# Optimization experiments

Hardware: AMD Instinct MI355X
Metric: run time of the kernel (lower is better)

Reference implementation:

```python
import jax, jax.numpy as jnp
import numpy as np


def ste_sign(w):
    # straight-through binarization: forward sign(w), backward identity
    return w + jax.lax.stop_gradient(jnp.sign(w) - w)


def spike(x):
    # Heaviside spike with straight-through estimator
    return x + jax.lax.stop_gradient((x > 0).astype(x.dtype) - x)


def quantized_conv1d(x, w, b, stride, padding):
    # XNOR-Net style 1-bit weights: sign(w) * per-out-channel mean(|w|)
    alpha = jnp.mean(jnp.abs(w), axis=(1, 2), keepdims=True)  # (O,1,1)
    wq = ste_sign(w) * alpha
    y = jax.lax.conv_general_dilated(
        x, wq, window_strides=(stride,), padding=[(padding, padding)],
        dimension_numbers=('NCH', 'OIH', 'NCH'))
    return y + b[None, :, None]


def batchnorm(x, gamma, beta, eps=1e-5):
    # training-mode BN over (batch, length) per channel
    mu = jnp.mean(x, axis=(0, 2), keepdims=True)
    var = jnp.var(x, axis=(0, 2), keepdims=True)
    return (x - mu) * jax.lax.rsqrt(var + eps) * gamma[None, :, None] + beta[None, :, None]


def window_attn(sq, sk, sv, w):
    # spiking attention restricted to non-overlapping windows of size w
    B, L, C = sq.shape
    pad = (-L) % w
    p = lambda a: jnp.pad(a, ((0, 0), (0, pad), (0, 0)))  # zero-pad -> zero spikes
    q = p(sq).reshape(B, -1, w, C)
    k = p(sk).reshape(B, -1, w, C)
    v = p(sv).reshape(B, -1, w, C)
    attn = jnp.einsum('bnwc,bnuc->bnwu', q, k)           # (B, nW, w, w)
    out = jnp.einsum('bnwu,bnuc->bnwc', attn, v) / w
    return out.reshape(B, -1, C)[:, :L]


def global_attn(sq, K, V, g):
    # pool K,V down to g global tokens, then linear spiking attention
    B, L, C = K.shape
    chunk = -(-L // g)
    pad = chunk * g - L
    p = lambda a: jnp.pad(a, ((0, 0), (0, pad), (0, 0)))
    kp = p(K).reshape(B, g, chunk, C).mean(axis=2)       # (B, g, C)
    vp = p(V).reshape(B, g, chunk, C).mean(axis=2)
    skg, svg = spike(kp), spike(vp)
    kv = jnp.einsum('bgc,bgd->bcd', skg, svg)            # (B, C, C)
    return jnp.einsum('blc,bcd->bld', sq, kv) / g


def mssa(x, wq, wk, wv, wo, local_w=64, regional_w=256, global_pool=16):
    # x: (B, C, L) -> token-major (B, L, C)
    h = jnp.swapaxes(x, 1, 2)
    Q, K, V = h @ wq, h @ wk, h @ wv
    sq, sk, sv = spike(Q), spike(K), spike(V)
    out = (window_attn(sq, sk, sv, local_w)
           + window_attn(sq, sk, sv, regional_w)
           + global_attn(sq, K, V, global_pool)) / 3.0
    y = h + out @ wo  # residual
    return jnp.swapaxes(y, 1, 2)


def setup_inputs() -> dict:
    key = jax.random.key(0)
    ks = jax.random.split(key, 8)
    B, Cin, L, Cout = 32, 256, 5000, 128
    return {
        'x': jax.random.normal(ks[0], (B, Cin, L), jnp.float32),
        'conv_w': jax.random.normal(ks[1], (Cout, Cin, 9), jnp.float32) * 0.05,
        'conv_b': jnp.zeros((Cout,), jnp.float32),
        'gamma': jnp.ones((Cout,), jnp.float32),
        'beta': jnp.zeros((Cout,), jnp.float32),
        'wq': jax.random.normal(ks[2], (Cout, Cout), jnp.float32) * 0.09,
        'wk': jax.random.normal(ks[3], (Cout, Cout), jnp.float32) * 0.09,
        'wv': jax.random.normal(ks[4], (Cout, Cout), jnp.float32) * 0.09,
        'wo': jax.random.normal(ks[5], (Cout, Cout), jnp.float32) * 0.09,
    }


def reference(x, conv_w, conv_b, gamma, beta, wq, wk, wv, wo):
    y = quantized_conv1d(x, conv_w, conv_b, stride=2, padding=4)  # (B,128,2500)
    y = jax.nn.elu(batchnorm(y, gamma, beta))
    return mssa(y, wq, wk, wv, wo)                                # (B,128,2500)
```

## Files before the change

### kernel.cpp

```cpp
#include <hip/hip_runtime.h>

typedef __attribute__((ext_vector_type(8))) short bf16x8;
typedef __attribute__((ext_vector_type(4))) float f32x4;
typedef __attribute__((ext_vector_type(16))) float f32x16;
typedef __attribute__((ext_vector_type(4))) unsigned int u32x4;
typedef __attribute__((ext_vector_type(4))) int s32x4;
typedef unsigned short u16;
typedef unsigned int u32;

#define DI __device__ __forceinline__

constexpr int B_ = 32, CI = 256, LX = 5000, CO = 128, LO = 2500, KW = 9, LP = 2560;

DI float b2f(u16 u) { u32 x = ((u32)u) << 16; return __builtin_bit_cast(float, x); }
DI u16 f2b(float f) {
  u32 x = __builtin_bit_cast(u32, f);
  u32 r = (x + 0x7fffu + ((x >> 16) & 1u)) >> 16;
  return (u16)r;
}
DI float elu(float v) { return v > 0.f ? v : expm1f(v); }

__global__ __launch_bounds__(256) void k_prep(const float* __restrict__ w, const float* __restrict__ wq,
                                              const float* __restrict__ wk, const float* __restrict__ wv,
                                              const float* __restrict__ wo, u16* __restrict__ wfmt,
                                              float* __restrict__ alphaf, u16* __restrict__ wThi,
                                              u16* __restrict__ wTlo, u16* __restrict__ wT3) {
  if (blockIdx.x < 128) {
    int o = blockIdx.x;
    const float* wrow = w + o * CI * KW;
    float s = 0.f;
    for (int idx = threadIdx.x; idx < CI * KW; idx += 256) s += fabsf(wrow[idx]);
    __shared__ float red[256];
    red[threadIdx.x] = s;
    __syncthreads();
    for (int st = 128; st > 0; st >>= 1) {
      if (threadIdx.x < st) red[threadIdx.x] += red[threadIdx.x + st];
      __syncthreads();
    }
    if (threadIdx.x == 0) alphaf[o] = red[0] / (float)(CI * KW);
    for (int idx = threadIdx.x; idx < CI * KW; idx += 256) {
      int i = idx / KW, k = idx - i * KW;
      float v = wrow[idx];
      float sg = v > 0.f ? 1.f : (v < 0.f ? -1.f : 0.f);
      wfmt[(((k * 16) + (i >> 4)) * 128 + o) * 16 + (i & 15)] = f2b(sg);
    }
  } else {
    const float* src[4] = {wq, wk, wv, wo};
    int mat = blockIdx.x - 128;
    const float* m = src[mat];
    u16* dh = wThi + mat * CO * CO;
    u16* dl = wTlo + mat * CO * CO;
    for (int idx = threadIdx.x; idx < CO * CO; idx += 256) {
      int nn = idx >> 7, kkn = idx & 127;
      float v = m[kkn * CO + nn];
      u16 hi = f2b(v);
      u16 lo = f2b(v - b2f(hi));
      dh[idx] = hi;
      dl[idx] = lo;
      if (mat < 3) {
        int nt = nn >> 4, n = nn & 15, ks = kkn >> 5, gj = kkn & 31;
        size_t base = (size_t)((mat * 4 + ks) * 8 + nt) * 1024 + n * 32 + gj;
        wT3[base] = hi;
        wT3[base + 512] = lo;
      }
    }
  }
}

__global__ __launch_bounds__(256) void k_conv(const float* __restrict__ x, const u16* __restrict__ wfmt,
                                              const float* __restrict__ bias, const float* __restrict__ alphaf,
                                              float* __restrict__ y1) {
  const int ltile = blockIdx.x, b = blockIdx.y;
  const int l0 = ltile * 32;
  const int lin0 = 2 * l0 - 4;
  alignas(16) __shared__ u16 xsh[72 * 136];
  alignas(16) __shared__ u16 xsl[72 * 136];
  const int tid = threadIdx.x;
  const int wave = tid >> 6, lane = tid & 63;
  const int col = lane & 31, g = lane >> 5;
  const int o0 = wave * 32;
  f32x16 acch = {};
  f32x16 accl = {};
  for (int cpass = 0; cpass < 2; ++cpass) {
    const int c0 = cpass * 128;
    if (cpass) __syncthreads();
#pragma unroll
    for (int it = 0; it < 9; ++it) {
      int idx = tid + it * 256;
      int i = idx / 18, q = idx - i * 18;
      int lin = lin0 + q * 4;
      const float* xr = x + ((size_t)(b * CI + c0 + i)) * LX;
      float4 v4 = float4{0.f, 0.f, 0.f, 0.f};
      if (lin >= 0 && lin + 4 <= LX) v4 = *reinterpret_cast<const float4*>(xr + lin);
      const float* vp = reinterpret_cast<const float*>(&v4);
#pragma unroll
      for (int e = 0; e < 4; ++e) {
        int p = q * 4 + e;
        float v = vp[e];
        u16 hi = f2b(v);
        int colx = ((((i >> 3) ^ ((p >> 1) & 15)) & 15) << 3) | (i & 7);
        xsh[p * 136 + colx] = hi;
        xsl[p * 136 + colx] = f2b(v - b2f(hi));
      }
    }
    __syncthreads();
    for (int kk = 0; kk < KW; ++kk) {
      bf16x8 af[8];
#pragma unroll
      for (int icg = 0; icg < 8; ++icg) {
        int chunk = kk * 16 + cpass * 8 + icg;
        af[icg] = *reinterpret_cast<const bf16x8*>(wfmt + ((size_t)chunk * 128 + o0 + col) * 16 + g * 8);
      }
      const int p = 2 * col + kk;
      const int prow = p * 136;
      const int s = (p >> 1) & 15;
#pragma unroll
      for (int icg = 0; icg < 8; ++icg) {
        int blkoff = (((icg * 2 + g) ^ s) << 3);
        bf16x8 bh = *reinterpret_cast<const bf16x8*>(&xsh[prow + blkoff]);
        bf16x8 bl = *reinterpret_cast<const bf16x8*>(&xsl[prow + blkoff]);
        acch = __builtin_amdgcn_mfma_f32_32x32x16_bf16(af[icg], bh, acch, 0, 0, 0);
        accl = __builtin_amdgcn_mfma_f32_32x32x16_bf16(af[icg], bl, accl, 0, 0, 0);
      }
    }
  }
  const int l = l0 + col;
  if (l < LO) {
#pragma unroll
    for (int r = 0; r < 16; ++r) {
      int o = o0 + (r & 3) + 8 * (r >> 2) + 4 * g;
      y1[(b * CO + o) * LO + l] = alphaf[o] * (acch[r] + accl[r]) + bias[o];
    }
  }
}

__global__ __launch_bounds__(256) void k_stats(const float* __restrict__ y1, float* __restrict__ ps,
                                               float* __restrict__ ps2) {
  int o = blockIdx.x, b = blockIdx.y;
  const float4* row = reinterpret_cast<const float4*>(y1 + (size_t)(b * CO + o) * LO);
  float s = 0.f, s2 = 0.f;
  for (int i = threadIdx.x; i < 625; i += 256) {
    float4 v = row[i];
    s += v.x + v.y + v.z + v.w;
    s2 += v.x * v.x + v.y * v.y + v.z * v.z + v.w * v.w;
  }
  __shared__ float r1[256], r2[256];
  r1[threadIdx.x] = s;
  r2[threadIdx.x] = s2;
  __syncthreads();
  for (int st = 128; st > 0; st >>= 1) {
    if (threadIdx.x < st) {
      r1[threadIdx.x] += r1[threadIdx.x + st];
      r2[threadIdx.x] += r2[threadIdx.x + st];
    }
    __syncthreads();
  }
  if (threadIdx.x == 0) {
    ps[b * CO + o] = r1[0];
    ps2[b * CO + o] = r2[0];
  }
}

__global__ void k_bnparams(const float* __restrict__ ps, const float* __restrict__ ps2,
                           const float* __restrict__ gamma, const float* __restrict__ beta,
                           float* __restrict__ bnsc, float* __restrict__ bnsh) {
  int o = threadIdx.x;
  float s = 0.f, s2 = 0.f;
  for (int b = 0; b < B_; ++b) {
    s += ps[b * CO + o];
    s2 += ps2[b * CO + o];
  }
  const float inv_n = 1.f / (float)(B_ * LO);
  float mu = s * inv_n;
  float var = s2 * inv_n - mu * mu;
  float sc = gamma[o] * rsqrtf(var + 1e-5f);
  bnsc[o] = sc;
  bnsh[o] = beta[o] - mu * sc;
}

__global__ __launch_bounds__(256) void k_qkv(const float* __restrict__ y1, const float* __restrict__ bnsc,
                                             const float* __restrict__ bnsh, const u16* __restrict__ wT3,
                                             signed char* __restrict__ sq8, signed char* __restrict__ sk8,
                                             u16* __restrict__ sv) {
  int tile = blockIdx.x, b = blockIdx.y;
  int tid = threadIdx.x, wave = tid >> 6, lane = tid & 63, n = lane & 15, g = lane >> 4;
  const int t0 = tile * 64;
  alignas(16) __shared__ u16 hshi[64 * 136];
  alignas(16) __shared__ u16 hslo[64 * 136];
  {
    int t = tid & 63;
    int l = t0 + t;
    if (l > LO - 1) l = LO - 1;
    for (int c = (tid >> 6); c < CO; c += 4) {
      float raw = y1[((size_t)b * CO + c) * LO + l];
      float e = elu(raw * bnsc[c] + bnsh[c]);
      u16 hi = f2b(e);
      hshi[t * 136 + c] = hi;
      hslo[t * 136 + c] = f2b(e - b2f(hi));
    }
  }
  __syncthreads();
  const u16* ah = &hshi[(wave * 16 + n) * 136];
  const u16* al = &hslo[(wave * 16 + n) * 136];
  for (int mat = 0; mat < 3; ++mat) {
    f32x4 acc[8] = {};
#pragma unroll
    for (int ks = 0; ks < 4; ++ks) {
      bf16x8 ahi = *reinterpret_cast<const bf16x8*>(ah + ks * 32 + g * 8);
      bf16x8 alo = *reinterpret_cast<const bf16x8*>(al + ks * 32 + g * 8);
      const u16* wbase = wT3 + (size_t)((mat * 4 + ks) * 8) * 1024 + n * 32 + g * 8;
#pragma unroll
      for (int nt = 0; nt < 8; ++nt) {
        bf16x8 bhi = *reinterpret_cast<const bf16x8*>(wbase + nt * 1024);
        bf16x8 blo = *reinterpret_cast<const bf16x8*>(wbase + nt * 1024 + 512);
        acc[nt] = __builtin_amdgcn_mfma_f32_16x16x32_bf16(ahi, bhi, acc[nt], 0, 0, 0);
        acc[nt] = __builtin_amdgcn_mfma_f32_16x16x32_bf16(ahi, blo, acc[nt], 0, 0, 0);
        acc[nt] = __builtin_amdgcn_mfma_f32_16x16x32_bf16(alo, bhi, acc[nt], 0, 0, 0);
        acc[nt] = __builtin_amdgcn_mfma_f32_16x16x32_bf16(alo, blo, acc[nt], 0, 0, 0);
      }
    }
#pragma unroll
    for (int nt = 0; nt < 8; ++nt) {
#pragma unroll
      for (int r = 0; r < 4; ++r) {
        int tok = t0 + wave * 16 + g * 4 + r;
        int c = nt * 16 + n;
        bool valid = tok < LO;
        float v = valid ? acc[nt][r] : 0.f;
        size_t oidx = ((size_t)b * LP + tok) * CO + c;
        if (mat == 2) {
          sv[oidx] = f2b(v > 0.f ? 1.f : 0.f);
        } else {
          signed char* so8 = (mat == 0) ? sq8 : sk8;
          so8[oidx] = v > 0.f ? 1 : 0;
        }
      }
    }
  }
}

__global__ __launch_bounds__(64) void k_poolh(const float* __restrict__ y1, const float* __restrict__ bnsc,
                                              const float* __restrict__ bnsh, float* __restrict__ hsum) {
  int c = blockIdx.x, b = blockIdx.y, lane = threadIdx.x;
  const float* row = y1 + ((size_t)b * CO + c) * LO;
  const float sc = bnsc[c], sh = bnsh[c];
  __shared__ float bins[16][64];
#pragma unroll
  for (int ch = 0; ch < 16; ++ch) bins[ch][lane] = 0.f;
  for (int j = lane; j < LO; j += 64) {
    float e = elu(row[j] * sc + sh);
    bins[j / 157][lane] += e;
  }
#pragma unroll
  for (int ch = 0; ch < 16; ++ch) {
    float v = bins[ch][lane];
    for (int off = 32; off > 0; off >>= 1) v += __shfl_down(v, off);
    if (lane == 0) hsum[(b * 16 + ch) * CO + c] = v;
  }
}

__global__ __launch_bounds__(256) void k_kv2(const float* __restrict__ hsum, const float* __restrict__ wk,
                                             const float* __restrict__ wv, signed char* __restrict__ kv8) {
  int b = blockIdx.x;
  __shared__ float hs[16 * 128], sks[16 * 128], svs[16 * 128];
  for (int i = threadIdx.x; i < 2048; i += 256) hs[i] = hsum[b * 2048 + i];
  __syncthreads();
  for (int idx = threadIdx.x; idx < 2048; idx += 256) {
    int gg = idx >> 7, c = idx & 127;
    float ak = 0.f, av = 0.f;
    for (int k = 0; k < 128; ++k) {
      float hv = hs[gg * 128 + k];
      ak += hv * wk[k * CO + c];
      av += hv * wv[k * CO + c];
    }
    sks[idx] = ak > 0.f ? 1.f : 0.f;
    svs[idx] = av > 0.f ? 1.f : 0.f;
  }
  __syncthreads();
  for (int idx = threadIdx.x; idx < CO * CO; idx += 256) {
    int d = idx >> 7, c = idx & 127;
    float s = 0.f;
#pragma unroll
    for (int gg = 0; gg < 16; ++gg) s += sks[gg * 128 + c] * svs[gg * 128 + d];
    kv8[b * CO * CO + idx] = (signed char)s;
  }
}

__global__ __launch_bounds__(512) void k_attn(const signed char* __restrict__ sq8,
                                              const signed char* __restrict__ sk8,
                                              const u16* __restrict__ sv, const signed char* __restrict__ kv8,
                                              const u16* __restrict__ woT, const float* __restrict__ y1,
                                              const float* __restrict__ bnsc, const float* __restrict__ bnsh,
                                              float* __restrict__ out) {
  const int win = blockIdx.x, b = blockIdx.y, qt = blockIdx.z;
  const int T0 = win * 256;
  alignas(16) __shared__ char smem[69632];
  u16* svT = reinterpret_cast<u16*>(smem);
  const int tid = threadIdx.x, wave = tid >> 6, lane = tid & 63, n = lane & 15, g = lane >> 4;
  for (int idx = tid; idx < 256 * 128; idx += 512) {
    int u = idx >> 7, c = idx & 127;
    svT[c * 264 + u] = sv[((size_t)b * LP + T0 + u) * CO + c];
  }
  __syncthreads();
  {
    const int qbase = wave * 32 + qt * 16;
    s32x4 bq8[2];
    const signed char* qrow = sq8 + ((size_t)b * LP + T0 + qbase + n) * CO;
    bq8[0] = *reinterpret_cast<const s32x4*>(qrow + g * 16);
    bq8[1] = *reinterpret_cast<const s32x4*>(qrow + 64 + g * 16);
    s32x4 pacc[16];
#pragma unroll
    for (int ut = 0; ut < 16; ++ut) pacc[ut] = s32x4{0, 0, 0, 0};
    for (int ut = 0; ut < 16; ++ut) {
      const signed char* krow = sk8 + ((size_t)b * LP + T0 + ut * 16 + n) * CO;
      s32x4 kf0 = *reinterpret_cast<const s32x4*>(krow + g * 16);
      s32x4 kf1 = *reinterpret_cast<const s32x4*>(krow + 64 + g * 16);
      pacc[ut] = __builtin_amdgcn_mfma_i32_16x16x64_i8(kf0, bq8[0], pacc[ut], 0, 0, 0);
      pacc[ut] = __builtin_amdgcn_mfma_i32_16x16x64_i8(kf1, bq8[1], pacc[ut], 0, 0, 0);
    }
    const int qblk = (qbase + n) >> 6;
    u32 packed[16][2];
#pragma unroll
    for (int ut = 0; ut < 16; ++ut) {
      u16 pk[4];
#pragma unroll
      for (int r = 0; r < 4; ++r) {
        int uloc = ut * 16 + g * 4 + r;
        float wgt = (1.f / 768.f) + (((uloc >> 6) == qblk) ? (1.f / 192.f) : 0.f);
        pk[r] = f2b((float)pacc[ut][r] * wgt);
      }
      packed[ut][0] = (u32)pk[0] | ((u32)pk[1] << 16);
      packed[ut][1] = (u32)pk[2] | ((u32)pk[3] << 16);
    }
    f32x4 acco[8];
#pragma unroll
    for (int ct = 0; ct < 8; ++ct) {
      s32x4 ag = {0, 0, 0, 0};
      const signed char* kvrow = kv8 + ((size_t)b * CO + ct * 16 + n) * CO;
      s32x4 k0 = *reinterpret_cast<const s32x4*>(kvrow + g * 16);
      s32x4 k1 = *reinterpret_cast<const s32x4*>(kvrow + 64 + g * 16);
      ag = __builtin_amdgcn_mfma_i32_16x16x64_i8(bq8[0], k0, ag, 0, 0, 0);
      ag = __builtin_amdgcn_mfma_i32_16x16x64_i8(bq8[1], k1, ag, 0, 0, 0);
#pragma unroll
      for (int r = 0; r < 4; ++r) acco[ct][r] = (float)ag[r] * (1.f / 48.f);
    }
    const int sl0 = n + 16 * ((g & 1) * 2);
    const int sl1 = sl0 + 16;
    const bool ghi = ((g >> 1) & 1) != 0;
#pragma unroll
    for (int us = 0; us < 8; ++us) {
      u32 a0e = (u32)__shfl((int)packed[us * 2][0], sl0, 64);
      u32 a0o = (u32)__shfl((int)packed[us * 2 + 1][0], sl0, 64);
      u32 a1e = (u32)__shfl((int)packed[us * 2][1], sl0, 64);
      u32 a1o = (u32)__shfl((int)packed[us * 2 + 1][1], sl0, 64);
      u32 a2e = (u32)__shfl((int)packed[us * 2][0], sl1, 64);
      u32 a2o = (u32)__shfl((int)packed[us * 2 + 1][0], sl1, 64);
      u32 a3e = (u32)__shfl((int)packed[us * 2][1], sl1, 64);
      u32 a3o = (u32)__shfl((int)packed[us * 2 + 1][1], sl1, 64);
      u32x4 paw = {ghi ? a0o : a0e, ghi ? a1o : a1e, ghi ? a2o : a2e, ghi ? a3o : a3e};
      bf16x8 pa = __builtin_bit_cast(bf16x8, paw);
#pragma unroll
      for (int ct = 0; ct < 8; ++ct) {
        bf16x8 bv = *reinterpret_cast<const bf16x8*>(&svT[(ct * 16 + n) * 264 + us * 32 + g * 8]);
        acco[ct] = __builtin_amdgcn_mfma_f32_16x16x32_bf16(pa, bv, acco[ct], 0, 0, 0);
      }
    }
    __syncthreads();
    u16* pw2 = reinterpret_cast<u16*>(smem) + wave * (16 * 136);
    float* sF = reinterpret_cast<float*>(smem + 34816) + wave * (64 * 17);
#pragma unroll
    for (int ct = 0; ct < 8; ++ct) {
#pragma unroll
      for (int r = 0; r < 4; ++r) {
        pw2[(g * 4 + r) * 136 + ct * 16 + n] = f2b(acco[ct][r]);
      }
    }
    for (int half = 0; half < 2; ++half) {
#pragma unroll
      for (int ot2 = 0; ot2 < 4; ++ot2) {
        int ot = half * 4 + ot2;
        f32x4 facc = {};
#pragma unroll
        for (int ks = 0; ks < 4; ++ks) {
          bf16x8 af = *reinterpret_cast<const bf16x8*>(&pw2[n * 136 + ks * 32 + g * 8]);
          bf16x8 bw = *reinterpret_cast<const bf16x8*>(&woT[(ot * 16 + n) * CO + ks * 32 + g * 8]);
          facc = __builtin_amdgcn_mfma_f32_16x16x32_bf16(af, bw, facc, 0, 0, 0);
        }
#pragma unroll
        for (int r = 0; r < 4; ++r) sF[(ot2 * 16 + n) * 17 + g * 4 + r] = facc[r];
      }
#pragma unroll
      for (int oo = 0; oo < 16; ++oo) {
        int olocal = oo * 4 + (lane >> 4);
        int o = half * 64 + olocal;
        int l = T0 + qbase + (lane & 15);
        float v = sF[olocal * 17 + (lane & 15)];
        if (l < LO) {
          size_t idx = ((size_t)b * CO + o) * LO + l;
          out[idx] = elu(y1[idx] * bnsc[o] + bnsh[o]) + v;
        }
      }
    }
  }
}

extern "C" void kernel_launch(void* const* d_in, const int* in_sizes, int n_in, void* d_out, int out_size,
                              void* d_ws, size_t ws_size, hipStream_t stream) {
  const float* x = (const float*)d_in[0];
  const float* conv_w = (const float*)d_in[1];
  const float* conv_b = (const float*)d_in[2];
  const float* gamma = (const float*)d_in[3];
  const float* beta = (const float*)d_in[4];
  const float* wq = (const float*)d_in[5];
  const float* wk = (const float*)d_in[6];
  const float* wv = (const float*)d_in[7];
  const float* wo = (const float*)d_in[8];
  (void)in_sizes; (void)n_in; (void)out_size; (void)ws_size;

  char* ws = (char*)d_ws;
  size_t off = 0;
  auto alloc = [&](size_t bytes) -> void* {
    void* p = ws + off;
    off += (bytes + 511) & ~(size_t)511;
    return p;
  };
  float* ps = (float*)alloc((size_t)B_ * CO * 4);
  float* ps2 = (float*)alloc((size_t)B_ * CO * 4);
  float* bnsc = (float*)alloc(CO * 4);
  float* bnsh = (float*)alloc(CO * 4);
  float* alphaf = (float*)alloc(CO * 4);
  float* hsum = (float*)alloc((size_t)B_ * 16 * CO * 4);
  signed char* kv8 = (signed char*)alloc((size_t)B_ * CO * CO);
  u16* wfmt = (u16*)alloc((size_t)CO * KW * CI * 2);
  u16* wThi = (u16*)alloc((size_t)4 * CO * CO * 2);
  u16* wTlo = (u16*)alloc((size_t)4 * CO * CO * 2);
  u16* wT3 = (u16*)alloc((size_t)3 * 4 * 8 * 1024 * 2);
  float* y1 = (float*)alloc((size_t)B_ * CO * LO * 4);
  signed char* sqb8 = (signed char*)alloc((size_t)B_ * LP * CO);
  signed char* skb8 = (signed char*)alloc((size_t)B_ * LP * CO);
  u16* svb = (u16*)alloc((size_t)B_ * LP * CO * 2);

  hipLaunchKernelGGL(k_prep, dim3(132), dim3(256), 0, stream, conv_w, wq, wk, wv, wo, wfmt, alphaf, wThi,
                     wTlo, wT3);
  hipLaunchKernelGGL(k_conv, dim3(80, B_), dim3(256), 0, stream, x, wfmt, conv_b, alphaf, y1);
  hipLaunchKernelGGL(k_stats, dim3(CO, B_), dim3(256), 0, stream, y1, ps, ps2);
  hipLaunchKernelGGL(k_bnparams, dim3(1), dim3(CO), 0, stream, ps, ps2, gamma, beta, bnsc, bnsh);
  hipLaunchKernelGGL(k_qkv, dim3(40, B_), dim3(256), 0, stream, y1, bnsc, bnsh, wT3, sqb8, skb8, svb);
  hipLaunchKernelGGL(k_poolh, dim3(CO, B_), dim3(64), 0, stream, y1, bnsc, bnsh, hsum);
  hipLaunchKernelGGL(k_kv2, dim3(B_), dim3(256), 0, stream, hsum, wk, wv, kv8);
  hipLaunchKernelGGL(k_attn, dim3(10, B_, 2), dim3(512), 0, stream, sqb8, skb8, svb, kv8, wThi + 3 * CO * CO,
                     y1, bnsc, bnsh, (float*)d_out);
}
```

Measured before the change: 427.1 us.

## Widen conv per-wave output tile and store V spikes as int8

```diff
diff --git a/kernel.cpp b/kernel.cpp
--- a/kernel.cpp
+++ b/kernel.cpp
@@ -67,7 +67,7 @@
   }
 }
 
-__global__ __launch_bounds__(256) void k_conv(const float* __restrict__ x, const u16* __restrict__ wfmt,
+__global__ __launch_bounds__(128) void k_conv(const float* __restrict__ x, const u16* __restrict__ wfmt,
                                               const float* __restrict__ bias, const float* __restrict__ alphaf,
                                               float* __restrict__ y1) {
   const int ltile = blockIdx.x, b = blockIdx.y;
@@ -78,15 +78,14 @@
   const int tid = threadIdx.x;
   const int wave = tid >> 6, lane = tid & 63;
   const int col = lane & 31, g = lane >> 5;
-  const int o0 = wave * 32;
-  f32x16 acch = {};
-  f32x16 accl = {};
+  const int o0 = wave * 64;
+  f32x16 acch0 = {}, accl0 = {}, acch1 = {}, accl1 = {};
   for (int cpass = 0; cpass < 2; ++cpass) {
     const int c0 = cpass * 128;
     if (cpass) __syncthreads();
 #pragma unroll
-    for (int it = 0; it < 9; ++it) {
-      int idx = tid + it * 256;
+    for (int it = 0; it < 18; ++it) {
+      int idx = tid + it * 128;
       int i = idx / 18, q = idx - i * 18;
       int lin = lin0 + q * 4;
       const float* xr = x + ((size_t)(b * CI + c0 + i)) * LX;
@@ -105,11 +104,12 @@
     }
     __syncthreads();
     for (int kk = 0; kk < KW; ++kk) {
-      bf16x8 af[8];
+      bf16x8 af0[8], af1[8];
 #pragma unroll
       for (int icg = 0; icg < 8; ++icg) {
         int chunk = kk * 16 + cpass * 8 + icg;
-        af[icg] = *reinterpret_cast<const bf16x8*>(wfmt + ((size_t)chunk * 128 + o0 + col) * 16 + g * 8);
+        af0[icg] = *reinterpret_cast<const bf16x8*>(wfmt + ((size_t)chunk * 128 + o0 + col) * 16 + g * 8);
+        af1[icg] = *reinterpret_cast<const bf16x8*>(wfmt + ((size_t)chunk * 128 + o0 + 32 + col) * 16 + g * 8);
       }
       const int p = 2 * col + kk;
       const int prow = p * 136;
@@ -119,8 +119,10 @@
         int blkoff = (((icg * 2 + g) ^ s) << 3);
         bf16x8 bh = *reinterpret_cast<const bf16x8*>(&xsh[prow + blkoff]);
         bf16x8 bl = *reinterpret_cast<const bf16x8*>(&xsl[prow + blkoff]);
-        acch = __builtin_amdgcn_mfma_f32_32x32x16_bf16(af[icg], bh, acch, 0, 0, 0);
-        accl = __builtin_amdgcn_mfma_f32_32x32x16_bf16(af[icg], bl, accl, 0, 0, 0);
+        acch0 = __builtin_amdgcn_mfma_f32_32x32x16_bf16(af0[icg], bh, acch0, 0, 0, 0);
+        accl0 = __builtin_amdgcn_mfma_f32_32x32x16_bf16(af0[icg], bl, accl0, 0, 0, 0);
+        acch1 = __builtin_amdgcn_mfma_f32_32x32x16_bf16(af1[icg], bh, acch1, 0, 0, 0);
+        accl1 = __builtin_amdgcn_mfma_f32_32x32x16_bf16(af1[icg], bl, accl1, 0, 0, 0);
       }
     }
   }
@@ -128,8 +130,10 @@
   if (l < LO) {
 #pragma unroll
     for (int r = 0; r < 16; ++r) {
-      int o = o0 + (r & 3) + 8 * (r >> 2) + 4 * g;
-      y1[(b * CO + o) * LO + l] = alphaf[o] * (acch[r] + accl[r]) + bias[o];
+      int orow = (r & 3) + 8 * (r >> 2) + 4 * g;
+      int oA = o0 + orow, oB = o0 + 32 + orow;
+      y1[(b * CO + oA) * LO + l] = alphaf[oA] * (acch0[r] + accl0[r]) + bias[oA];
+      y1[(b * CO + oB) * LO + l] = alphaf[oB] * (acch1[r] + accl1[r]) + bias[oB];
     }
   }
 }
@@ -181,7 +185,7 @@
 __global__ __launch_bounds__(256) void k_qkv(const float* __restrict__ y1, const float* __restrict__ bnsc,
                                              const float* __restrict__ bnsh, const u16* __restrict__ wT3,
                                              signed char* __restrict__ sq8, signed char* __restrict__ sk8,
-                                             u16* __restrict__ sv) {
+                                             signed char* __restrict__ sv8) {
   int tile = blockIdx.x, b = blockIdx.y;
   int tid = threadIdx.x, wave = tid >> 6, lane = tid & 63, n = lane & 15, g = lane >> 4;
   const int t0 = tile * 64;
@@ -202,6 +206,7 @@
   __syncthreads();
   const u16* ah = &hshi[(wave * 16 + n) * 136];
   const u16* al = &hslo[(wave * 16 + n) * 136];
+  signed char* outs[3] = {sq8, sk8, sv8};
   for (int mat = 0; mat < 3; ++mat) {
     f32x4 acc[8] = {};
 #pragma unroll
@@ -219,6 +224,7 @@
         acc[nt] = __builtin_amdgcn_mfma_f32_16x16x32_bf16(alo, blo, acc[nt], 0, 0, 0);
       }
     }
+    signed char* so = outs[mat];
 #pragma unroll
     for (int nt = 0; nt < 8; ++nt) {
 #pragma unroll
@@ -227,13 +233,7 @@
         int c = nt * 16 + n;
         bool valid = tok < LO;
         float v = valid ? acc[nt][r] : 0.f;
-        size_t oidx = ((size_t)b * LP + tok) * CO + c;
-        if (mat == 2) {
-          sv[oidx] = f2b(v > 0.f ? 1.f : 0.f);
-        } else {
-          signed char* so8 = (mat == 0) ? sq8 : sk8;
-          so8[oidx] = v > 0.f ? 1 : 0;
-        }
+        so[((size_t)b * LP + tok) * CO + c] = v > 0.f ? 1 : 0;
       }
     }
   }
@@ -288,7 +288,8 @@
 
 __global__ __launch_bounds__(512) void k_attn(const signed char* __restrict__ sq8,
                                               const signed char* __restrict__ sk8,
-                                              const u16* __restrict__ sv, const signed char* __restrict__ kv8,
+                                              const signed char* __restrict__ sv8,
+                                              const signed char* __restrict__ kv8,
                                               const u16* __restrict__ woT, const float* __restrict__ y1,
                                               const float* __restrict__ bnsc, const float* __restrict__ bnsh,
                                               float* __restrict__ out) {
@@ -297,9 +298,13 @@
   alignas(16) __shared__ char smem[69632];
   u16* svT = reinterpret_cast<u16*>(smem);
   const int tid = threadIdx.x, wave = tid >> 6, lane = tid & 63, n = lane & 15, g = lane >> 4;
-  for (int idx = tid; idx < 256 * 128; idx += 512) {
-    int u = idx >> 7, c = idx & 127;
-    svT[c * 264 + u] = sv[((size_t)b * LP + T0 + u) * CO + c];
+  for (int i = tid; i < 8192; i += 512) {
+    int u = i >> 5, c4 = (i & 31) << 2;
+    u32 w4 = *reinterpret_cast<const u32*>(sv8 + ((size_t)b * LP + T0 + u) * CO + c4);
+#pragma unroll
+    for (int j = 0; j < 4; ++j) {
+      svT[(c4 + j) * 264 + u] = ((w4 >> (8 * j)) & 0xffu) ? (u16)0x3F80 : (u16)0;
+    }
   }
   __syncthreads();
   {
@@ -438,16 +443,16 @@
   float* y1 = (float*)alloc((size_t)B_ * CO * LO * 4);
   signed char* sqb8 = (signed char*)alloc((size_t)B_ * LP * CO);
   signed char* skb8 = (signed char*)alloc((size_t)B_ * LP * CO);
-  u16* svb = (u16*)alloc((size_t)B_ * LP * CO * 2);
+  signed char* svb8 = (signed char*)alloc((size_t)B_ * LP * CO);
 
   hipLaunchKernelGGL(k_prep, dim3(132), dim3(256), 0, stream, conv_w, wq, wk, wv, wo, wfmt, alphaf, wThi,
                      wTlo, wT3);
-  hipLaunchKernelGGL(k_conv, dim3(80, B_), dim3(256), 0, stream, x, wfmt, conv_b, alphaf, y1);
+  hipLaunchKernelGGL(k_conv, dim3(80, B_), dim3(128), 0, stream, x, wfmt, conv_b, alphaf, y1);
   hipLaunchKernelGGL(k_stats, dim3(CO, B_), dim3(256), 0, stream, y1, ps, ps2);
   hipLaunchKernelGGL(k_bnparams, dim3(1), dim3(CO), 0, stream, ps, ps2, gamma, beta, bnsc, bnsh);
-  hipLaunchKernelGGL(k_qkv, dim3(40, B_), dim3(256), 0, stream, y1, bnsc, bnsh, wT3, sqb8, skb8, svb);
+  hipLaunchKernelGGL(k_qkv, dim3(40, B_), dim3(256), 0, stream, y1, bnsc, bnsh, wT3, sqb8, skb8, svb8);
   hipLaunchKernelGGL(k_poolh, dim3(CO, B_), dim3(64), 0, stream, y1, bnsc, bnsh, hsum);
   hipLaunchKernelGGL(k_kv2, dim3(B_), dim3(256), 0, stream, hsum, wk, wv, kv8);
-  hipLaunchKernelGGL(k_attn, dim3(10, B_, 2), dim3(512), 0, stream, sqb8, skb8, svb, kv8, wThi + 3 * CO * CO,
+  hipLaunchKernelGGL(k_attn, dim3(10, B_, 2), dim3(512), 0, stream, sqb8, skb8, svb8, kv8, wThi + 3 * CO * CO,
                      y1, bnsc, bnsh, (float*)d_out);
 }
```

New measurement: 473.2 us. +10.8%, slower.
